# Kernel optimization log

Measured on AMD Instinct MI355X. Metric: run time of the kernel, lower is better.

The kernel has to match this reference:

```python
import jax, jax.numpy as jnp
import numpy as np

HID, H, KV, S, B = 2048, 32, 8, 2048, 2
D = HID // H           # head_dim = 64
G = H // KV            # query heads per kv head = 4


def setup_inputs() -> dict:
    key = jax.random.key(0)
    ks = jax.random.split(key, 10)
    sc = 0.02
    kv_dim = HID * KV // H  # 512
    return {
        "x": jax.random.normal(ks[0], (B, S, HID), jnp.float32),
        "attention_mask": jnp.zeros((B, S), jnp.float32),
        "Wq": jax.random.normal(ks[1], (HID, HID), jnp.float32) * sc,
        "bq": jnp.zeros((HID,), jnp.float32),
        "Wk": jax.random.normal(ks[2], (kv_dim, HID), jnp.float32) * sc,
        "bk": jnp.zeros((kv_dim,), jnp.float32),
        "Wv": jax.random.normal(ks[3], (kv_dim, HID), jnp.float32) * sc,
        "bv": jnp.zeros((kv_dim,), jnp.float32),
        "Wo": jax.random.normal(ks[4], (HID, HID), jnp.float32) * sc,
        "bo": jnp.zeros((HID,), jnp.float32),
    }


def reference(x, attention_mask, Wq, bq, Wk, bk, Wv, bv, Wo, bo):
    Bx, Sx, _ = x.shape
    # projections (torch Linear: x @ W.T + b)
    q = x @ Wq.T + bq                                  # [B,S,HID]
    k = x @ Wk.T + bk                                  # [B,S,KV*D]
    v = x @ Wv.T + bv
    # split heads: [B,S,H,D] -> [B,H,S,D]; then group q: [B,KV,G,S,D]
    q = q.reshape(Bx, Sx, H, D).transpose(0, 2, 1, 3).reshape(Bx, KV, G, Sx, D)
    k = k.reshape(Bx, Sx, KV, D).transpose(0, 2, 1, 3)  # [B,KV,S,D]
    v = v.reshape(Bx, Sx, KV, D).transpose(0, 2, 1, 3)
    scale = 1.0 / jnp.sqrt(jnp.float32(D))
    scores = jnp.einsum('bkgsd,bktd->bkgst', q, k) * scale  # [B,KV,G,S,S]
    scores = scores + attention_mask[:, None, None, None, :]
    attn = jax.nn.softmax(scores, axis=-1)
    out = jnp.einsum('bkgst,bktd->bkgsd', attn, v)          # [B,KV,G,S,D]
    out = out.reshape(Bx, H, Sx, D).transpose(0, 2, 1, 3).reshape(Bx, Sx, HID)
    return out @ Wo.T + bo
```

## Files before the change

### kernel.cpp

```cpp
#include <hip/hip_runtime.h>
#include <hip/hip_bf16.h>
#include <stdint.h>

typedef __hip_bfloat16 bf16;
typedef __attribute__((ext_vector_type(8))) short bf16x8;
typedef __attribute__((ext_vector_type(4))) float f32x4;
typedef __attribute__((ext_vector_type(16))) float f32x16;
typedef __attribute__((ext_vector_type(4))) int i32x4;
typedef __attribute__((ext_vector_type(2))) int i32x2;

#define B_   2
#define S_   2048
#define HID_ 2048
#define H_   32
#define KV_  8
#define D_   64
#define NT_  (S_ / 64)
#define LOG2E 1.4426950408889634f

__device__ __forceinline__ void gload_lds16(const void* g, void* l) {
  __builtin_amdgcn_global_load_lds(
      (const __attribute__((address_space(1))) uint32_t*)g,
      (__attribute__((address_space(3))) uint32_t*)l, 16, 0, 0);
}
__device__ __forceinline__ float fexp2(float x) { return __builtin_amdgcn_exp2f(x); }

__device__ __forceinline__ uint32_t cvtpk_bf16(float lo, float hi) {
  uint32_t r;
  asm("v_cvt_pk_bf16_f32 %0, %1, %2" : "=v"(r) : "v"(lo), "v"(hi));
  return r;
}
__device__ __forceinline__ void plane32_swap(uint32_t& a, uint32_t& b) {
  i32x2 r = __builtin_amdgcn_permlane32_swap((int)a, (int)b, false, false);
  a = (uint32_t)r[0]; b = (uint32_t)r[1];
}

__global__ __launch_bounds__(256) void cvt_f32_bf16(
    const float* __restrict__ s, bf16* __restrict__ d, int n4) {
  int i = blockIdx.x * blockDim.x + threadIdx.x;
  const int stride = gridDim.x * blockDim.x;
  for (; i < n4; i += stride) {
    float4 v = ((const float4*)s)[i];
    bf16 t[4];
    t[0] = __float2bfloat16(v.x);
    t[1] = __float2bfloat16(v.y);
    t[2] = __float2bfloat16(v.z);
    t[3] = __float2bfloat16(v.w);
    *reinterpret_cast<uint64_t*>(d + 4 * (size_t)i) = *reinterpret_cast<uint64_t*>(t);
  }
}

__global__ __launch_bounds__(256) void mask_prep(
    const float* __restrict__ m, float* __restrict__ o, int n) {
  int i = blockIdx.x * blockDim.x + threadIdx.x;
  if (i < n) o[i] = m[i] * LOG2E;
}

__global__ __launch_bounds__(256, 2) void gemm_qkv(
    const bf16* __restrict__ A,
    const bf16* __restrict__ Wqp, const bf16* __restrict__ Wkp, const bf16* __restrict__ Wvp,
    const float* __restrict__ bqp, const float* __restrict__ bkp, const float* __restrict__ bvp,
    bf16* __restrict__ Cq, bf16* __restrict__ Ck, bf16* __restrict__ Cv) {
  const int lid0 = blockIdx.y * gridDim.x + blockIdx.x;
  const int q8 = (int)(gridDim.x * gridDim.y) >> 3;
  const int lid = (lid0 & 7) * q8 + (lid0 >> 3);
  const int bm = lid & 31;
  const int bn_all = lid >> 5;

  const bf16* W; const float* bias; int bn;
  if (bn_all < 16)      { W = Wqp; bias = bqp; bn = bn_all; }
  else if (bn_all < 20) { W = Wkp; bias = bkp; bn = bn_all - 16; }
  else                  { W = Wvp; bias = bvp; bn = bn_all - 20; }
  const float oscale = (bn_all < 16) ? (0.125f * LOG2E) : 1.0f;

  __shared__ __align__(16) bf16 As[128 * 64];
  __shared__ __align__(16) bf16 Bs[128 * 64];
  const int tid = threadIdx.x;
  const int lane = tid & 63, wid = tid >> 6;
  const int wr = wid >> 1, wc = wid & 1;
  const int K = HID_;

  f32x4 acc[4][4] = {};

  for (int k0 = 0; k0 < K; k0 += 64) {
    __syncthreads();
#pragma unroll
    for (int c = 0; c < 4; ++c) {
      const int r = c * 32 + wid * 8 + (lane >> 3);
      const int gcolb = ((lane & 7) * 16) ^ ((r & 7) << 4);
      gload_lds16(A + (size_t)(bm * 128 + r) * K + k0 + (gcolb >> 1),
                  &As[(c * 32 + wid * 8) * 64]);
      gload_lds16(W + (size_t)(bn * 128 + r) * K + k0 + (gcolb >> 1),
                  &Bs[(c * 32 + wid * 8) * 64]);
    }
    __syncthreads();
#pragma unroll
    for (int ks = 0; ks < 2; ++ks) {
      bf16x8 af[4], bfr[4];
#pragma unroll
      for (int i = 0; i < 4; ++i) {
        const int ra = wr * 64 + i * 16 + (lane & 15);
        const int ka = (ks * 64 + ((lane >> 4) << 4)) ^ ((ra & 7) << 4);
        af[i] = *(const bf16x8*)((const char*)As + ra * 128 + ka);
        const int rb = wc * 64 + i * 16 + (lane & 15);
        const int kb = (ks * 64 + ((lane >> 4) << 4)) ^ ((rb & 7) << 4);
        bfr[i] = *(const bf16x8*)((const char*)Bs + rb * 128 + kb);
      }
      __builtin_amdgcn_s_setprio(1);
#pragma unroll
      for (int i = 0; i < 4; ++i)
#pragma unroll
        for (int j = 0; j < 4; ++j)
          acc[i][j] = __builtin_amdgcn_mfma_f32_16x16x32_bf16(af[i], bfr[j], acc[i][j], 0, 0, 0);
      __builtin_amdgcn_s_setprio(0);
    }
  }

  if (bn_all < 20) {
    const int Hn = (bn_all < 16) ? H_ : KV_;
    bf16* C = (bn_all < 16) ? Cq : Ck;
#pragma unroll
    for (int j = 0; j < 4; ++j) {
      const int n = bn * 128 + wc * 64 + j * 16 + (lane & 15);
      const float bv = bias[n];
#pragma unroll
      for (int i = 0; i < 4; ++i) {
        const int mb = bm * 128 + wr * 64 + i * 16 + ((lane >> 4) << 2);
#pragma unroll
        for (int e = 0; e < 4; ++e) {
          const int m = mb + e;
          const float v = (acc[i][j][e] + bv) * oscale;
          const int b = m >> 11, s = m & (S_ - 1);
          const int h = n >> 6, d = n & 63;
          C[(((size_t)b * Hn + h) * S_ + s) * 64 + d] = __float2bfloat16(v);
        }
      }
    }
  } else {
#pragma unroll
    for (int j = 0; j < 4; ++j) {
      const int n = bn * 128 + wc * 64 + j * 16 + (lane & 15);
      const int kvh = n >> 6, d = n & 63;
      const float bv = bias[n];
#pragma unroll
      for (int i = 0; i < 4; ++i) {
        const int m0 = bm * 128 + wr * 64 + i * 16 + ((lane >> 4) << 2);
        const int b = m0 >> 11, s0 = m0 & (S_ - 1);
        bf16 t4[4];
#pragma unroll
        for (int e = 0; e < 4; ++e) t4[e] = __float2bfloat16(acc[i][j][e] + bv);
        *reinterpret_cast<uint64_t*>(
            Cv + (((size_t)b * KV_ + kvh) * D_ + d) * S_ + s0) =
            *reinterpret_cast<uint64_t*>(t4);
      }
    }
  }
}

__global__ __launch_bounds__(256, 2) void gemm_out(
    const bf16* __restrict__ A, const bf16* __restrict__ W,
    const float* __restrict__ bias, float* __restrict__ C) {
  const int lid0 = blockIdx.y * gridDim.x + blockIdx.x;
  const int q8 = (int)(gridDim.x * gridDim.y) >> 3;
  const int lid = (lid0 & 7) * q8 + (lid0 >> 3);
  const int bm = lid & 31;
  const int bn = lid >> 5;

  __shared__ __align__(16) bf16 As[128 * 64];
  __shared__ __align__(16) bf16 Bs[128 * 64];
  const int tid = threadIdx.x;
  const int lane = tid & 63, wid = tid >> 6;
  const int wr = wid >> 1, wc = wid & 1;
  const int K = HID_, N = HID_;

  f32x4 acc[4][4] = {};

  for (int k0 = 0; k0 < K; k0 += 64) {
    __syncthreads();
#pragma unroll
    for (int c = 0; c < 4; ++c) {
      const int r = c * 32 + wid * 8 + (lane >> 3);
      const int gcolb = ((lane & 7) * 16) ^ ((r & 7) << 4);
      gload_lds16(A + (size_t)(bm * 128 + r) * K + k0 + (gcolb >> 1),
                  &As[(c * 32 + wid * 8) * 64]);
      gload_lds16(W + (size_t)(bn * 128 + r) * K + k0 + (gcolb >> 1),
                  &Bs[(c * 32 + wid * 8) * 64]);
    }
    __syncthreads();
#pragma unroll
    for (int ks = 0; ks < 2; ++ks) {
      bf16x8 af[4], bfr[4];
#pragma unroll
      for (int i = 0; i < 4; ++i) {
        const int ra = wr * 64 + i * 16 + (lane & 15);
        const int ka = (ks * 64 + ((lane >> 4) << 4)) ^ ((ra & 7) << 4);
        af[i] = *(const bf16x8*)((const char*)As + ra * 128 + ka);
        const int rb = wc * 64 + i * 16 + (lane & 15);
        const int kb = (ks * 64 + ((lane >> 4) << 4)) ^ ((rb & 7) << 4);
        bfr[i] = *(const bf16x8*)((const char*)Bs + rb * 128 + kb);
      }
      __builtin_amdgcn_s_setprio(1);
#pragma unroll
      for (int i = 0; i < 4; ++i)
#pragma unroll
        for (int j = 0; j < 4; ++j)
          acc[i][j] = __builtin_amdgcn_mfma_f32_16x16x32_bf16(af[i], bfr[j], acc[i][j], 0, 0, 0);
      __builtin_amdgcn_s_setprio(0);
    }
  }

#pragma unroll
  for (int j = 0; j < 4; ++j) {
    const int n = bn * 128 + wc * 64 + j * 16 + (lane & 15);
    const float bv = bias[n];
#pragma unroll
    for (int i = 0; i < 4; ++i) {
      const int mb = bm * 128 + wr * 64 + i * 16 + ((lane >> 4) << 2);
#pragma unroll
      for (int e = 0; e < 4; ++e) {
        C[(size_t)(mb + e) * N + n] = acc[i][j][e] + bv;
      }
    }
  }
}

__global__ __launch_bounds__(256, 4) void attn_fwd(
    const bf16* __restrict__ qb, const bf16* __restrict__ kb,
    const bf16* __restrict__ vtb, const float* __restrict__ maskL,
    bf16* __restrict__ ob) {
  const int lid0 = blockIdx.y * gridDim.x + blockIdx.x;
  const int q8 = (int)(gridDim.x * gridDim.y) >> 3;
  const int lid = (lid0 & 7) * q8 + (lid0 >> 3);
  const int qtile = lid & 15;
  const int headid = lid >> 4;
  const int b = headid >> 5, h = headid & (H_ - 1);
  const int kv = h >> 2;
  const int tid = threadIdx.x, lane = tid & 63, wid = tid >> 6;
  const int l31 = lane & 31, hi = lane >> 5;

  __shared__ __align__(16) bf16 Ks[2][64 * 64];
  __shared__ __align__(16) bf16 VTs[2][64 * 64];
  __shared__ float lsm[4][32];

  const bf16* qh = qb + ((size_t)(b * H_ + h) * S_) * D_;
  const bf16* kh = kb + ((size_t)(b * KV_ + kv) * S_) * D_;
  const bf16* vth = vtb + (size_t)(b * KV_ + kv) * D_ * S_;
  const float* mrow = maskL + (size_t)b * S_;

  const int qrow = qtile * 128 + wid * 32 + l31;
  bf16x8 qf[4];
#pragma unroll
  for (int ks = 0; ks < 4; ++ks)
    qf[ks] = *(const bf16x8*)(qh + (size_t)qrow * D_ + ks * 16 + hi * 8);

  float lp = 0.f;
  f32x16 o[2] = {};

#pragma unroll
  for (int c = 0; c < 2; ++c) {
    const int r = c * 32 + wid * 8 + (lane >> 3);
    const int gcolb = ((lane & 7) * 16) ^ ((r & 7) << 4);
    gload_lds16(kh + (size_t)r * D_ + (gcolb >> 1), &Ks[0][(c * 32 + wid * 8) * 64]);
    gload_lds16(vth + (size_t)r * S_ + (gcolb >> 1), &VTs[0][(c * 32 + wid * 8) * 64]);
  }
  __syncthreads();

  for (int t = 0; t < NT_; ++t) {
    const int cur = t & 1, nxt = cur ^ 1;

    if (t < NT_ - 1) {
#pragma unroll
      for (int c = 0; c < 2; ++c) {
        const int r = c * 32 + wid * 8 + (lane >> 3);
        const int gcolb = ((lane & 7) * 16) ^ ((r & 7) << 4);
        gload_lds16(kh + ((size_t)(t + 1) * 64 + r) * D_ + (gcolb >> 1),
                    &Ks[nxt][(c * 32 + wid * 8) * 64]);
        gload_lds16(vth + (size_t)r * S_ + (t + 1) * 64 + (gcolb >> 1),
                    &VTs[nxt][(c * 32 + wid * 8) * 64]);
      }
    }

    f32x16 s[2];
#pragma unroll
    for (int kbv = 0; kbv < 2; ++kbv) {
#pragma unroll
      for (int rq = 0; rq < 4; ++rq) {
        const f32x4 m4 = *(const f32x4*)(mrow + t * 64 + kbv * 32 + rq * 8 + 4 * hi);
#pragma unroll
        for (int e = 0; e < 4; ++e) s[kbv][rq * 4 + e] = m4[e];
      }
    }
#pragma unroll
    for (int kbv = 0; kbv < 2; ++kbv) {
      __builtin_amdgcn_s_setprio(1);
#pragma unroll
      for (int ks = 0; ks < 4; ++ks) {
        const int rk = kbv * 32 + l31;
        const int kbyte = (ks * 32 + hi * 16) ^ ((rk & 7) << 4);
        bf16x8 kf = *(const bf16x8*)((const char*)&Ks[cur][0] + rk * 128 + kbyte);
        s[kbv] = __builtin_amdgcn_mfma_f32_32x32x16_bf16(kf, qf[ks], s[kbv], 0, 0, 0);
      }
      __builtin_amdgcn_s_setprio(0);
    }

    float2 ps2 = make_float2(0.f, 0.f);
#pragma unroll
    for (int kbv = 0; kbv < 2; ++kbv)
#pragma unroll
      for (int r8 = 0; r8 < 8; ++r8) {
        const float pa_ = fexp2(s[kbv][2 * r8]);
        const float pb_ = fexp2(s[kbv][2 * r8 + 1]);
        s[kbv][2 * r8] = pa_;
        s[kbv][2 * r8 + 1] = pb_;
        ps2.x += pa_;
        ps2.y += pb_;
      }
    lp += ps2.x + ps2.y;

    bf16x8 pa[2][2];
#pragma unroll
    for (int kbv = 0; kbv < 2; ++kbv) {
      uint32_t a0 = cvtpk_bf16(s[kbv][0], s[kbv][1]);
      uint32_t b0 = cvtpk_bf16(s[kbv][4], s[kbv][5]);
      plane32_swap(a0, b0);
      uint32_t a1 = cvtpk_bf16(s[kbv][2], s[kbv][3]);
      uint32_t b1 = cvtpk_bf16(s[kbv][6], s[kbv][7]);
      plane32_swap(a1, b1);
      i32x4 t0; t0[0] = (int)a0; t0[1] = (int)a1; t0[2] = (int)b0; t0[3] = (int)b1;
      pa[kbv][0] = __builtin_bit_cast(bf16x8, t0);
      uint32_t a2 = cvtpk_bf16(s[kbv][8], s[kbv][9]);
      uint32_t b2 = cvtpk_bf16(s[kbv][12], s[kbv][13]);
      plane32_swap(a2, b2);
      uint32_t a3 = cvtpk_bf16(s[kbv][10], s[kbv][11]);
      uint32_t b3 = cvtpk_bf16(s[kbv][14], s[kbv][15]);
      plane32_swap(a3, b3);
      i32x4 t1; t1[0] = (int)a2; t1[1] = (int)a3; t1[2] = (int)b2; t1[3] = (int)b3;
      pa[kbv][1] = __builtin_bit_cast(bf16x8, t1);
    }

#pragma unroll
    for (int db = 0; db < 2; ++db) {
      __builtin_amdgcn_s_setprio(1);
#pragma unroll
      for (int kbv = 0; kbv < 2; ++kbv)
#pragma unroll
        for (int ks2 = 0; ks2 < 2; ++ks2) {
          const int rd = db * 32 + l31;
          const int vbyte = (kbv * 64 + ks2 * 32 + hi * 16) ^ ((rd & 7) << 4);
          bf16x8 vf = *(const bf16x8*)((const char*)&VTs[cur][0] + rd * 128 + vbyte);
          o[db] = __builtin_amdgcn_mfma_f32_32x32x16_bf16(pa[kbv][ks2], vf, o[db], 0, 0, 0);
        }
      __builtin_amdgcn_s_setprio(0);
    }

    __syncthreads();
  }

  {
    uint32_t la = __float_as_uint(lp), lb = la;
    plane32_swap(la, lb);
    const float lsum = __uint_as_float(la) + __uint_as_float(lb);
    lsm[wid][l31] = lsum;
  }
  __syncthreads();
#pragma unroll
  for (int rq = 0; rq < 4; ++rq) {
    const f32x4 l4 = *(const f32x4*)&lsm[wid][rq * 8 + 4 * hi];
#pragma unroll
    for (int e2 = 0; e2 < 4; ++e2) {
      const float inv = 1.0f / l4[e2];
      const int q_out = e2 + 8 * rq + 4 * hi;
      const int srow = qtile * 128 + wid * 32 + q_out;
#pragma unroll
      for (int db = 0; db < 2; ++db) {
        const float val = o[db][rq * 4 + e2] * inv;
        ob[((size_t)b * S_ + srow) * HID_ + h * 64 + db * 32 + l31] = __float2bfloat16(val);
      }
    }
  }
}

extern "C" void kernel_launch(void* const* d_in, const int* in_sizes, int n_in,
                              void* d_out, int out_size, void* d_ws, size_t ws_size,
                              hipStream_t stream) {
  (void)in_sizes; (void)n_in; (void)out_size; (void)ws_size;
  const float* x  = (const float*)d_in[0];
  const float* am = (const float*)d_in[1];
  const float* Wq = (const float*)d_in[2];
  const float* bq = (const float*)d_in[3];
  const float* Wk = (const float*)d_in[4];
  const float* bk = (const float*)d_in[5];
  const float* Wv = (const float*)d_in[6];
  const float* bv = (const float*)d_in[7];
  const float* Wo = (const float*)d_in[8];
  const float* bo = (const float*)d_in[9];
  float* out = (float*)d_out;

  const size_t XE  = (size_t)B_ * S_ * HID_;
  const size_t WQE = (size_t)HID_ * HID_;
  const size_t WKE = (size_t)(KV_ * D_) * HID_;
  const size_t QE  = (size_t)B_ * H_ * S_ * D_;
  const size_t KE  = (size_t)B_ * KV_ * S_ * D_;

  bf16* xb  = (bf16*)d_ws;
  bf16* wqb = xb + XE;
  bf16* wkb = wqb + WQE;
  bf16* wvb = wkb + WKE;
  bf16* wob = wvb + WKE;
  bf16* qbuf = wob + WQE;
  bf16* kbuf = qbuf + QE;
  bf16* vtbuf = kbuf + KE;
  bf16* abuf = vtbuf + KE;
  float* maskL = (float*)(abuf + XE);

  dim3 blk(256);
  cvt_f32_bf16<<<2048, blk, 0, stream>>>(x,  xb,  (int)(XE / 4));
  cvt_f32_bf16<<<2048, blk, 0, stream>>>(Wq, wqb, (int)(WQE / 4));
  cvt_f32_bf16<<<1024, blk, 0, stream>>>(Wk, wkb, (int)(WKE / 4));
  cvt_f32_bf16<<<1024, blk, 0, stream>>>(Wv, wvb, (int)(WKE / 4));
  cvt_f32_bf16<<<2048, blk, 0, stream>>>(Wo, wob, (int)(WQE / 4));
  mask_prep<<<(B_ * S_ + 255) / 256, blk, 0, stream>>>(am, maskL, B_ * S_);

  const int M = B_ * S_;
  gemm_qkv<<<dim3(M / 128, 24), blk, 0, stream>>>(xb, wqb, wkb, wvb, bq, bk, bv,
                                                  qbuf, kbuf, vtbuf);
  attn_fwd<<<dim3(S_ / 128, B_ * H_), blk, 0, stream>>>(qbuf, kbuf, vtbuf, maskL, abuf);
  gemm_out<<<dim3(M / 128, HID_ / 128), blk, 0, stream>>>(abuf, wob, bo, out);
}
```

Before: 202.5 us.

## Double per-wave query rows in attention and merge conversion kernels into one launch

The attention kernel now has each wave handle 64 query rows instead of 32, so every K/V fragment read from LDS feeds two MFMA chains and each block covers 256 query rows. This halves the grid and the total K/V global and LDS traffic per output row, at the cost of more registers and a lower occupancy bound (launch bounds drop from 4 to 2). Separately, the five fp32-to-bf16 conversion launches are merged into one kernel that picks its job from blockIdx.y, which removes launch overhead.

```diff
diff --git a/kernel.cpp b/kernel.cpp
--- a/kernel.cpp
+++ b/kernel.cpp
@@ -35,18 +35,27 @@
   a = (uint32_t)r[0]; b = (uint32_t)r[1];
 }
 
-__global__ __launch_bounds__(256) void cvt_f32_bf16(
-    const float* __restrict__ s, bf16* __restrict__ d, int n4) {
+struct CvtJob { const float* s; bf16* d; int n4; };
+__global__ __launch_bounds__(256) void cvt_multi(
+    CvtJob j0, CvtJob j1, CvtJob j2, CvtJob j3, CvtJob j4) {
+  CvtJob j;
+  switch (blockIdx.y) {
+    case 0: j = j0; break;
+    case 1: j = j1; break;
+    case 2: j = j2; break;
+    case 3: j = j3; break;
+    default: j = j4; break;
+  }
   int i = blockIdx.x * blockDim.x + threadIdx.x;
   const int stride = gridDim.x * blockDim.x;
-  for (; i < n4; i += stride) {
-    float4 v = ((const float4*)s)[i];
+  for (; i < j.n4; i += stride) {
+    float4 v = ((const float4*)j.s)[i];
     bf16 t[4];
     t[0] = __float2bfloat16(v.x);
     t[1] = __float2bfloat16(v.y);
     t[2] = __float2bfloat16(v.z);
     t[3] = __float2bfloat16(v.w);
-    *reinterpret_cast<uint64_t*>(d + 4 * (size_t)i) = *reinterpret_cast<uint64_t*>(t);
+    *reinterpret_cast<uint64_t*>(j.d + 4 * (size_t)i) = *reinterpret_cast<uint64_t*>(t);
   }
 }
 
@@ -224,15 +233,15 @@
   }
 }
 
-__global__ __launch_bounds__(256, 4) void attn_fwd(
+__global__ __launch_bounds__(256, 2) void attn_fwd(
     const bf16* __restrict__ qb, const bf16* __restrict__ kb,
     const bf16* __restrict__ vtb, const float* __restrict__ maskL,
     bf16* __restrict__ ob) {
   const int lid0 = blockIdx.y * gridDim.x + blockIdx.x;
   const int q8 = (int)(gridDim.x * gridDim.y) >> 3;
   const int lid = (lid0 & 7) * q8 + (lid0 >> 3);
-  const int qtile = lid & 15;
-  const int headid = lid >> 4;
+  const int qtile = lid & 7;
+  const int headid = lid >> 3;
   const int b = headid >> 5, h = headid & (H_ - 1);
   const int kv = h >> 2;
   const int tid = threadIdx.x, lane = tid & 63, wid = tid >> 6;
@@ -240,21 +249,23 @@
 
   __shared__ __align__(16) bf16 Ks[2][64 * 64];
   __shared__ __align__(16) bf16 VTs[2][64 * 64];
-  __shared__ float lsm[4][32];
+  __shared__ float lsm[4][64];
 
   const bf16* qh = qb + ((size_t)(b * H_ + h) * S_) * D_;
   const bf16* kh = kb + ((size_t)(b * KV_ + kv) * S_) * D_;
   const bf16* vth = vtb + (size_t)(b * KV_ + kv) * D_ * S_;
   const float* mrow = maskL + (size_t)b * S_;
 
-  const int qrow = qtile * 128 + wid * 32 + l31;
-  bf16x8 qf[4];
-#pragma unroll
-  for (int ks = 0; ks < 4; ++ks)
-    qf[ks] = *(const bf16x8*)(qh + (size_t)qrow * D_ + ks * 16 + hi * 8);
-
-  float lp = 0.f;
-  f32x16 o[2] = {};
+  const int qrowbase = qtile * 256 + wid * 64;
+  bf16x8 qf[2][4];
+#pragma unroll
+  for (int qs = 0; qs < 2; ++qs)
+#pragma unroll
+    for (int ks = 0; ks < 4; ++ks)
+      qf[qs][ks] = *(const bf16x8*)(qh + (size_t)(qrowbase + qs * 32 + l31) * D_ + ks * 16 + hi * 8);
+
+  float lp0 = 0.f, lp1 = 0.f;
+  f32x16 o0[2] = {}, o1[2] = {};
 
 #pragma unroll
   for (int c = 0; c < 2; ++c) {
@@ -280,14 +291,17 @@
       }
     }
 
-    f32x16 s[2];
+    f32x16 s0[2], s1[2];
 #pragma unroll
     for (int kbv = 0; kbv < 2; ++kbv) {
 #pragma unroll
       for (int rq = 0; rq < 4; ++rq) {
         const f32x4 m4 = *(const f32x4*)(mrow + t * 64 + kbv * 32 + rq * 8 + 4 * hi);
 #pragma unroll
-        for (int e = 0; e < 4; ++e) s[kbv][rq * 4 + e] = m4[e];
+        for (int e = 0; e < 4; ++e) {
+          s0[kbv][rq * 4 + e] = m4[e];
+          s1[kbv][rq * 4 + e] = m4[e];
+        }
       }
     }
 #pragma unroll
@@ -298,44 +312,70 @@
         const int rk = kbv * 32 + l31;
         const int kbyte = (ks * 32 + hi * 16) ^ ((rk & 7) << 4);
         bf16x8 kf = *(const bf16x8*)((const char*)&Ks[cur][0] + rk * 128 + kbyte);
-        s[kbv] = __builtin_amdgcn_mfma_f32_32x32x16_bf16(kf, qf[ks], s[kbv], 0, 0, 0);
+        s0[kbv] = __builtin_amdgcn_mfma_f32_32x32x16_bf16(kf, qf[0][ks], s0[kbv], 0, 0, 0);
+        s1[kbv] = __builtin_amdgcn_mfma_f32_32x32x16_bf16(kf, qf[1][ks], s1[kbv], 0, 0, 0);
       }
       __builtin_amdgcn_s_setprio(0);
     }
 
-    float2 ps2 = make_float2(0.f, 0.f);
-#pragma unroll
-    for (int kbv = 0; kbv < 2; ++kbv)
-#pragma unroll
-      for (int r8 = 0; r8 < 8; ++r8) {
-        const float pa_ = fexp2(s[kbv][2 * r8]);
-        const float pb_ = fexp2(s[kbv][2 * r8 + 1]);
-        s[kbv][2 * r8] = pa_;
-        s[kbv][2 * r8 + 1] = pb_;
-        ps2.x += pa_;
-        ps2.y += pb_;
-      }
-    lp += ps2.x + ps2.y;
-
-    bf16x8 pa[2][2];
+    {
+      float2 a0 = make_float2(0.f, 0.f), a1 = make_float2(0.f, 0.f);
+#pragma unroll
+      for (int kbv = 0; kbv < 2; ++kbv)
+#pragma unroll
+        for (int r8 = 0; r8 < 8; ++r8) {
+          const float p00 = fexp2(s0[kbv][2 * r8]);
+          const float p01 = fexp2(s0[kbv][2 * r8 + 1]);
+          const float p10 = fexp2(s1[kbv][2 * r8]);
+          const float p11 = fexp2(s1[kbv][2 * r8 + 1]);
+          s0[kbv][2 * r8] = p00; s0[kbv][2 * r8 + 1] = p01;
+          s1[kbv][2 * r8] = p10; s1[kbv][2 * r8 + 1] = p11;
+          a0.x += p00; a0.y += p01;
+          a1.x += p10; a1.y += p11;
+        }
+      lp0 += a0.x + a0.y;
+      lp1 += a1.x + a1.y;
+    }
+
+    bf16x8 pa0[2][2], pa1[2][2];
 #pragma unroll
     for (int kbv = 0; kbv < 2; ++kbv) {
-      uint32_t a0 = cvtpk_bf16(s[kbv][0], s[kbv][1]);
-      uint32_t b0 = cvtpk_bf16(s[kbv][4], s[kbv][5]);
-      plane32_swap(a0, b0);
-      uint32_t a1 = cvtpk_bf16(s[kbv][2], s[kbv][3]);
-      uint32_t b1 = cvtpk_bf16(s[kbv][6], s[kbv][7]);
-      plane32_swap(a1, b1);
-      i32x4 t0; t0[0] = (int)a0; t0[1] = (int)a1; t0[2] = (int)b0; t0[3] = (int)b1;
-      pa[kbv][0] = __builtin_bit_cast(bf16x8, t0);
-      uint32_t a2 = cvtpk_bf16(s[kbv][8], s[kbv][9]);
-      uint32_t b2 = cvtpk_bf16(s[kbv][12], s[kbv][13]);
-      plane32_swap(a2, b2);
-      uint32_t a3 = cvtpk_bf16(s[kbv][10], s[kbv][11]);
-      uint32_t b3 = cvtpk_bf16(s[kbv][14], s[kbv][15]);
-      plane32_swap(a3, b3);
-      i32x4 t1; t1[0] = (int)a2; t1[1] = (int)a3; t1[2] = (int)b2; t1[3] = (int)b3;
-      pa[kbv][1] = __builtin_bit_cast(bf16x8, t1);
+      {
+        uint32_t a0 = cvtpk_bf16(s0[kbv][0], s0[kbv][1]);
+        uint32_t b0 = cvtpk_bf16(s0[kbv][4], s0[kbv][5]);
+        plane32_swap(a0, b0);
+        uint32_t a1 = cvtpk_bf16(s0[kbv][2], s0[kbv][3]);
+        uint32_t b1 = cvtpk_bf16(s0[kbv][6], s0[kbv][7]);
+        plane32_swap(a1, b1);
+        i32x4 t0; t0[0] = (int)a0; t0[1] = (int)a1; t0[2] = (int)b0; t0[3] = (int)b1;
+        pa0[kbv][0] = __builtin_bit_cast(bf16x8, t0);
+        uint32_t a2 = cvtpk_bf16(s0[kbv][8], s0[kbv][9]);
+        uint32_t b2 = cvtpk_bf16(s0[kbv][12], s0[kbv][13]);
+        plane32_swap(a2, b2);
+        uint32_t a3 = cvtpk_bf16(s0[kbv][10], s0[kbv][11]);
+        uint32_t b3 = cvtpk_bf16(s0[kbv][14], s0[kbv][15]);
+        plane32_swap(a3, b3);
+        i32x4 t1; t1[0] = (int)a2; t1[1] = (int)a3; t1[2] = (int)b2; t1[3] = (int)b3;
+        pa0[kbv][1] = __builtin_bit_cast(bf16x8, t1);
+      }
+      {
+        uint32_t a0 = cvtpk_bf16(s1[kbv][0], s1[kbv][1]);
+        uint32_t b0 = cvtpk_bf16(s1[kbv][4], s1[kbv][5]);
+        plane32_swap(a0, b0);
+        uint32_t a1 = cvtpk_bf16(s1[kbv][2], s1[kbv][3]);
+        uint32_t b1 = cvtpk_bf16(s1[kbv][6], s1[kbv][7]);
+        plane32_swap(a1, b1);
+        i32x4 t0; t0[0] = (int)a0; t0[1] = (int)a1; t0[2] = (int)b0; t0[3] = (int)b1;
+        pa1[kbv][0] = __builtin_bit_cast(bf16x8, t0);
+        uint32_t a2 = cvtpk_bf16(s1[kbv][8], s1[kbv][9]);
+        uint32_t b2 = cvtpk_bf16(s1[kbv][12], s1[kbv][13]);
+        plane32_swap(a2, b2);
+        uint32_t a3 = cvtpk_bf16(s1[kbv][10], s1[kbv][11]);
+        uint32_t b3 = cvtpk_bf16(s1[kbv][14], s1[kbv][15]);
+        plane32_swap(a3, b3);
+        i32x4 t1; t1[0] = (int)a2; t1[1] = (int)a3; t1[2] = (int)b2; t1[3] = (int)b3;
+        pa1[kbv][1] = __builtin_bit_cast(bf16x8, t1);
+      }
     }
 
 #pragma unroll
@@ -348,7 +388,8 @@
           const int rd = db * 32 + l31;
           const int vbyte = (kbv * 64 + ks2 * 32 + hi * 16) ^ ((rd & 7) << 4);
           bf16x8 vf = *(const bf16x8*)((const char*)&VTs[cur][0] + rd * 128 + vbyte);
-          o[db] = __builtin_amdgcn_mfma_f32_32x32x16_bf16(pa[kbv][ks2], vf, o[db], 0, 0, 0);
+          o0[db] = __builtin_amdgcn_mfma_f32_32x32x16_bf16(pa0[kbv][ks2], vf, o0[db], 0, 0, 0);
+          o1[db] = __builtin_amdgcn_mfma_f32_32x32x16_bf16(pa1[kbv][ks2], vf, o1[db], 0, 0, 0);
         }
       __builtin_amdgcn_s_setprio(0);
     }
@@ -357,24 +398,29 @@
   }
 
   {
-    uint32_t la = __float_as_uint(lp), lb = la;
+    uint32_t la = __float_as_uint(lp0), lb = la;
     plane32_swap(la, lb);
-    const float lsum = __uint_as_float(la) + __uint_as_float(lb);
-    lsm[wid][l31] = lsum;
+    lsm[wid][l31] = __uint_as_float(la) + __uint_as_float(lb);
+    uint32_t lc = __float_as_uint(lp1), ld = lc;
+    plane32_swap(lc, ld);
+    lsm[wid][32 + l31] = __uint_as_float(lc) + __uint_as_float(ld);
   }
   __syncthreads();
 #pragma unroll
-  for (int rq = 0; rq < 4; ++rq) {
-    const f32x4 l4 = *(const f32x4*)&lsm[wid][rq * 8 + 4 * hi];
-#pragma unroll
-    for (int e2 = 0; e2 < 4; ++e2) {
-      const float inv = 1.0f / l4[e2];
-      const int q_out = e2 + 8 * rq + 4 * hi;
-      const int srow = qtile * 128 + wid * 32 + q_out;
-#pragma unroll
-      for (int db = 0; db < 2; ++db) {
-        const float val = o[db][rq * 4 + e2] * inv;
-        ob[((size_t)b * S_ + srow) * HID_ + h * 64 + db * 32 + l31] = __float2bfloat16(val);
+  for (int qs = 0; qs < 2; ++qs) {
+#pragma unroll
+    for (int rq = 0; rq < 4; ++rq) {
+      const f32x4 l4 = *(const f32x4*)&lsm[wid][qs * 32 + rq * 8 + 4 * hi];
+#pragma unroll
+      for (int e2 = 0; e2 < 4; ++e2) {
+        const float inv = 1.0f / l4[e2];
+        const int q_out = e2 + 8 * rq + 4 * hi;
+        const int srow = qrowbase + qs * 32 + q_out;
+#pragma unroll
+        for (int db = 0; db < 2; ++db) {
+          const float val = (qs == 0 ? o0[db][rq * 4 + e2] : o1[db][rq * 4 + e2]) * inv;
+          ob[((size_t)b * S_ + srow) * HID_ + h * 64 + db * 32 + l31] = __float2bfloat16(val);
+        }
       }
     }
   }
@@ -414,16 +460,17 @@
   float* maskL = (float*)(abuf + XE);
 
   dim3 blk(256);
-  cvt_f32_bf16<<<2048, blk, 0, stream>>>(x,  xb,  (int)(XE / 4));
-  cvt_f32_bf16<<<2048, blk, 0, stream>>>(Wq, wqb, (int)(WQE / 4));
-  cvt_f32_bf16<<<1024, blk, 0, stream>>>(Wk, wkb, (int)(WKE / 4));
-  cvt_f32_bf16<<<1024, blk, 0, stream>>>(Wv, wvb, (int)(WKE / 4));
-  cvt_f32_bf16<<<2048, blk, 0, stream>>>(Wo, wob, (int)(WQE / 4));
+  CvtJob jx  = { x,  xb,  (int)(XE / 4) };
+  CvtJob jwq = { Wq, wqb, (int)(WQE / 4) };
+  CvtJob jwk = { Wk, wkb, (int)(WKE / 4) };
+  CvtJob jwv = { Wv, wvb, (int)(WKE / 4) };
+  CvtJob jwo = { Wo, wob, (int)(WQE / 4) };
+  cvt_multi<<<dim3(512, 5), blk, 0, stream>>>(jx, jwq, jwk, jwv, jwo);
   mask_prep<<<(B_ * S_ + 255) / 256, blk, 0, stream>>>(am, maskL, B_ * S_);
 
   const int M = B_ * S_;
   gemm_qkv<<<dim3(M / 128, 24), blk, 0, stream>>>(xb, wqb, wkb, wvb, bq, bk, bv,
                                                   qbuf, kbuf, vtbuf);
-  attn_fwd<<<dim3(S_ / 128, B_ * H_), blk, 0, stream>>>(qbuf, kbuf, vtbuf, maskL, abuf);
+  attn_fwd<<<dim3(S_ / 256, B_ * H_), blk, 0, stream>>>(qbuf, kbuf, vtbuf, maskL, abuf);
   gemm_out<<<dim3(M / 128, HID_ / 128), blk, 0, stream>>>(abuf, wob, bo, out);
 }
```

New measurement: 192.2 us. 1.05x faster.
